# Performance work log

Measured on AMD Instinct MI355X. Metric: run time of the kernel, lower is better.

Reference implementation:

```python
import jax, jax.numpy as jnp
import numpy as np

B, T, C, H = 128, 256, 512, 512

def setup_inputs() -> dict:
    key = jax.random.key(0)
    k1, k2, k3, k4 = jax.random.split(key, 4)
    x = jax.random.normal(k1, (B, T, C), dtype=jnp.float32)
    # nn.Linear(n_embed, H_size, bias=False).weight has shape [H, C]; scaled init
    s = 1.0 / np.sqrt(C)
    Wq = jax.random.normal(k2, (H, C), dtype=jnp.float32) * s
    Wk = jax.random.normal(k3, (H, C), dtype=jnp.float32) * s
    Wv = jax.random.normal(k4, (H, C), dtype=jnp.float32) * s
    return {"x": x, "Wq": Wq, "Wk": Wk, "Wv": Wv}

def reference(x, Wq, Wk, Wv):
    # q,k,v: [B,T,H] = x @ W.T (torch Linear convention)
    q = jnp.einsum('btc,hc->bth', x, Wq)
    k = jnp.einsum('btc,hc->bth', x, Wk)
    v = jnp.einsum('btc,hc->bth', x, Wv)
    scale = k.shape[-1] ** -0.5
    score = jnp.einsum('bqh,bkh->bqk', q, k) * scale  # [B,T,T]
    # causal mask: position j attends to i only if i <= j
    i = jnp.arange(T)
    causal = i[None, :] <= i[:, None]  # [T,T] lower-triangular
    score = jnp.where(causal[None, :, :], score, -jnp.inf)
    attn = jax.nn.softmax(score, axis=-1)
    # dropout is identity in eval mode
    out = jnp.einsum('bqk,bkh->bqh', attn, v)  # [B,T,H]
    return out
```

## Files before the change

### kernel.cpp

```cpp
#include <hip/hip_runtime.h>

#define B_ 128
#define T_ 256
#define C_ 512
#define H_ 512
#define CSCALE 0.063763824f

typedef _Float16 f16x8 __attribute__((ext_vector_type(8)));
typedef _Float16 f16x4 __attribute__((ext_vector_type(4)));
typedef _Float16 f16x2 __attribute__((ext_vector_type(2)));
typedef float    f32x4 __attribute__((ext_vector_type(4)));
typedef float    f32x16 __attribute__((ext_vector_type(16)));
typedef unsigned int u32;
typedef u32 u32x4 __attribute__((ext_vector_type(4)));

__device__ __forceinline__ void gld16(const void* gsrc, void* ldst) {
  __builtin_amdgcn_global_load_lds(
      (__attribute__((address_space(1))) void*)gsrc,
      (__attribute__((address_space(3))) void*)ldst, 16, 0, 0);
}

__global__ __launch_bounds__(256) void cvt_kernel(
    const float4* __restrict__ x, const float4* __restrict__ wq,
    const float4* __restrict__ wk, const float4* __restrict__ wv,
    f16x4* __restrict__ dst) {
  const int NX = (B_ * T_ * C_) / 4;
  const int NW = (H_ * C_) / 4;
  const int total = NX + 3 * NW;
  int gid = blockIdx.x * 256 + threadIdx.x;
  int gsz = gridDim.x * 256;
  for (int i = gid; i < total; i += gsz) {
    float4 f;
    if (i < NX)            f = x[i];
    else if (i < NX + NW)  f = wq[i - NX];
    else if (i < NX + 2*NW) f = wk[i - NX - NW];
    else                   f = wv[i - NX - 2*NW];
    f16x4 u = {(_Float16)f.x, (_Float16)f.y, (_Float16)f.z, (_Float16)f.w};
    dst[i] = u;
  }
}

__global__ __launch_bounds__(512, 2) void proj_kernel(
    const _Float16* __restrict__ xh, const _Float16* __restrict__ wh,
    _Float16* __restrict__ qh, _Float16* __restrict__ kh,
    _Float16* __restrict__ vth) {
  __shared__ _Float16 L[65536];

  const int tid  = threadIdx.x;
  const int lane = tid & 63;
  const int wave = tid >> 6;
  const int lr = lane & 15, lk = lane >> 4;
  const int lane8 = lane * 8;
  const int wr = wave >> 2, wc = wave & 3;
  const int m0 = blockIdx.x * 256;
  const int n0 = blockIdx.y * 256;
  const int z  = blockIdx.z;
  const _Float16* wz = wh + z * (H_ * C_);

  const int srow = wave * 16 + lr;
  const int scol = lk * 8;
  const _Float16* aS = xh + (size_t)(m0 + srow) * C_ + scol;
  const _Float16* bS = wz + (size_t)(n0 + srow) * C_ + scol;

  f32x4 acc[8][4];
#pragma unroll
  for (int i = 0; i < 8; ++i)
#pragma unroll
    for (int j = 0; j < 4; ++j) acc[i][j] = {0.f, 0.f, 0.f, 0.f};
  f16x8 af[4], bf[4];

  gld16(aS,               &L[(wave) * 512]);
  gld16(aS + 65536,       &L[(8 + wave) * 512]);
  gld16(bS,               &L[16384 + (wave) * 512]);
  gld16(bS + 65536,       &L[16384 + (8 + wave) * 512]);
  gld16(aS + 32,          &L[(16 + wave) * 512]);
  gld16(aS + 65536 + 32,  &L[(16 + 8 + wave) * 512]);
  gld16(bS + 32,          &L[16384 + (16 + wave) * 512]);
  gld16(bS + 65536 + 32,  &L[16384 + (16 + 8 + wave) * 512]);
  asm volatile("s_waitcnt vmcnt(4)" ::: "memory");
  __builtin_amdgcn_s_barrier();

#define PH(BUF, MH, KH, STK, SKK, SBUF, SB, VM) do {                          \
    if ((MH) == 0) {                                                           \
      _Pragma("unroll") for (int ni = 0; ni < 4; ++ni)                         \
        bf[ni] = *(const f16x8*)&L[(BUF) * 32768 + 16384 +                     \
                                   ((KH) * 16 + wc * 4 + ni) * 512 + lane8];   \
    }                                                                          \
    _Pragma("unroll") for (int q = 0; q < 4; ++q)                              \
      af[q] = *(const f16x8*)&L[(BUF) * 32768 +                                \
                                ((KH) * 16 + wr * 8 + (MH) * 4 + q) * 512 +    \
                                lane8];                                        \
    {                                                                          \
      const _Float16* s_ = (SB) ? bS : aS;                                     \
      const int db_ = (SBUF) * 32768 + ((SB) ? 16384 : 0);                     \
      gld16(s_ + (STK) + (SKK) * 32,                                           \
            &L[db_ + ((SKK) * 16 + wave) * 512]);                              \
      gld16(s_ + 65536 + (STK) + (SKK) * 32,                                   \
            &L[db_ + ((SKK) * 16 + 8 + wave) * 512]);                          \
    }                                                                          \
    __builtin_amdgcn_s_barrier();                                              \
    __builtin_amdgcn_s_setprio(1);                                             \
    _Pragma("unroll") for (int q = 0; q < 4; ++q)                              \
      _Pragma("unroll") for (int ni = 0; ni < 4; ++ni)                         \
        acc[(MH) * 4 + q][ni] = __builtin_amdgcn_mfma_f32_16x16x32_f16(        \
            af[q], bf[ni], acc[(MH) * 4 + q][ni], 0, 0, 0);                    \
    __builtin_amdgcn_s_setprio(0);                                             \
    if (VM) asm volatile("s_waitcnt vmcnt(4)" ::: "memory");                   \
    __builtin_amdgcn_s_barrier();                                              \
  } while (0)

#pragma unroll 1
  for (int it = 0; it < 4; ++it) {
    const int k1 = (2 * it + 1) * 64;
    const int k2 = (2 * it + 2 < 8 ? 2 * it + 2 : 7) * 64;
    PH(0, 0, 0, k1, 0, 1, 0, 0);
    PH(0, 1, 0, k1, 0, 1, 1, 1);
    PH(0, 0, 1, k1, 1, 1, 0, 0);
    PH(0, 1, 1, k1, 1, 1, 1, 1);
    PH(1, 0, 0, k2, 0, 0, 0, 0);
    PH(1, 1, 0, k2, 0, 0, 1, 1);
    PH(1, 0, 1, k2, 1, 0, 0, 0);
    PH(1, 1, 1, k2, 1, 0, 1, 1);
  }
#undef PH

  if (z < 2) {
    _Float16* out = (z == 0) ? qh : kh;
#pragma unroll
    for (int mi = 0; mi < 8; ++mi) {
      int mg = m0 + wr * 128 + mi * 16 + lk * 4;
#pragma unroll
      for (int ni = 0; ni < 4; ++ni) {
        int n = n0 + wc * 64 + ni * 16 + lr;
#pragma unroll
        for (int r = 0; r < 4; ++r)
          out[(size_t)(mg + r) * H_ + n] = (_Float16)acc[mi][ni][r];
      }
    }
  } else {
    int bb = m0 >> 8;
#pragma unroll
    for (int mi = 0; mi < 8; ++mi) {
      int ttb = wr * 128 + mi * 16 + lk * 4;
#pragma unroll
      for (int ni = 0; ni < 4; ++ni) {
        int n = n0 + wc * 64 + ni * 16 + lr;
        f16x4 u = {(_Float16)acc[mi][ni][0], (_Float16)acc[mi][ni][1],
                   (_Float16)acc[mi][ni][2], (_Float16)acc[mi][ni][3]};
        *(f16x4*)&vth[(size_t)bb * (H_ * T_) + (size_t)n * T_ + ttb] = u;
      }
    }
  }
}

__global__ __launch_bounds__(256, 2) void attn_kernel(
    const _Float16* __restrict__ qh, const _Float16* __restrict__ kh,
    const _Float16* __restrict__ vth, float* __restrict__ dout) {
  __shared__ f32x4 Ex[2][4][4][64];

  const int tid  = threadIdx.x;
  const int lane = tid & 63;
  const int wq   = tid >> 6;
  const int lq   = lane & 31;
  const int hi   = lane >> 5;
  const int flat = blockIdx.x;
  const int xcd  = flat & 7;
  const int rest = flat >> 3;
  const int qb   = 7 - (rest & 7);
  const int g    = rest >> 3;
  const int b    = xcd + (g << 3);
  const int q0   = qb * 32;
  const int nkv  = qb + 1;
  const int hbase = wq * 128;
  const int qg   = q0 + lq;

  f16x8 qf[8];
  const _Float16* qp = qh + ((size_t)b * T_ + qg) * H_ + hbase + hi * 8;
#pragma unroll
  for (int ks = 0; ks < 8; ++ks) qf[ks] = *(const f16x8*)&qp[ks * 16];

  f32x16 ot[4];
#pragma unroll
  for (int i = 0; i < 4; ++i) ot[i] = {};
  float m_ = -1e30f, l_ = 0.f;

  const _Float16* kp = kh  + ((size_t)b * T_ + lq) * H_ + hbase + hi * 8;
  const _Float16* vp = vth + ((size_t)b * H_ + hbase + lq) * T_ + hi * 8;

  for (int kvt = 0; kvt < nkv; ++kvt) {
    const int kv0 = kvt * 32;

    f16x8 kf[8];
#pragma unroll
    for (int ks = 0; ks < 8; ++ks)
      kf[ks] = *(const f16x8*)&kp[(size_t)kv0 * H_ + ks * 16];
    f32x16 st = {};
#pragma unroll
    for (int ks = 0; ks < 8; ++ks)
      st = __builtin_amdgcn_mfma_f32_32x32x16_f16(kf[ks], qf[ks], st, 0, 0, 0);

    const int buf = kvt & 1;
#pragma unroll
    for (int c = 0; c < 4; ++c) {
      f32x4 w4 = {st[c*4+0], st[c*4+1], st[c*4+2], st[c*4+3]};
      Ex[buf][wq][c][lane] = w4;
    }
    __syncthreads();
#pragma unroll
    for (int ow = 0; ow < 4; ++ow) {
      if (ow == wq) continue;
#pragma unroll
      for (int c = 0; c < 4; ++c) {
        f32x4 r4 = Ex[buf][ow][c][lane];
        st[c*4+0] += r4[0]; st[c*4+1] += r4[1];
        st[c*4+2] += r4[2]; st[c*4+3] += r4[3];
      }
    }

    float p[16], rm = -1e30f;
    const int kvb = kv0 + 4 * hi;
#pragma unroll
    for (int r = 0; r < 16; ++r) {
      int kvg = kvb + (r & 3) + 8 * (r >> 2);
      float v = (kvg > qg) ? -1e30f : st[r];
      p[r] = v;
      rm = fmaxf(rm, v);
    }
    rm = fmaxf(rm, __shfl_xor(rm, 32, 64));

    if (__any((int)(rm > m_ + 64.f))) {
      float mn = fmaxf(m_, rm);
      float al = __builtin_amdgcn_exp2f((m_ - mn) * CSCALE);
      m_ = mn; l_ *= al;
#pragma unroll
      for (int i = 0; i < 4; ++i)
#pragma unroll
        for (int e = 0; e < 16; ++e) ot[i][e] *= al;
    }
    float rs = 0.f;
#pragma unroll
    for (int r = 0; r < 16; ++r) {
      p[r] = __builtin_amdgcn_exp2f((p[r] - m_) * CSCALE);
      rs += p[r];
    }
    rs += __shfl_xor(rs, 32, 64);
    l_ += rs;

    u32 w[8], sw[8];
#pragma unroll
    for (int i = 0; i < 8; ++i) {
      f16x2 h2; h2[0] = (_Float16)p[2*i]; h2[1] = (_Float16)p[2*i+1];
      w[i] = __builtin_bit_cast(u32, h2);
    }
#pragma unroll
    for (int i = 0; i < 8; ++i) sw[i] = (u32)__shfl_xor((int)w[i], 32, 64);
    u32x4 t0 = { hi ? sw[2] : w[0],  hi ? sw[3] : w[1],
                 hi ? w[2]  : sw[0], hi ? w[3]  : sw[1] };
    u32x4 t1 = { hi ? sw[6] : w[4],  hi ? sw[7] : w[5],
                 hi ? w[6]  : sw[4], hi ? w[7]  : sw[5] };
    f16x8 pb0 = __builtin_bit_cast(f16x8, t0);
    f16x8 pb1 = __builtin_bit_cast(f16x8, t1);

#pragma unroll
    for (int ht = 0; ht < 4; ++ht) {
      f16x8 va0 = *(const f16x8*)&vp[(size_t)(ht * 32) * T_ + kv0];
      f16x8 va1 = *(const f16x8*)&vp[(size_t)(ht * 32) * T_ + kv0 + 16];
      ot[ht] = __builtin_amdgcn_mfma_f32_32x32x16_f16(va0, pb0, ot[ht], 0, 0, 0);
      ot[ht] = __builtin_amdgcn_mfma_f32_32x32x16_f16(va1, pb1, ot[ht], 0, 0, 0);
    }
  }

  float li = 1.0f / l_;
  float* op = dout + ((size_t)b * T_ + qg) * H_ + hbase + 4 * hi;
#pragma unroll
  for (int ht = 0; ht < 4; ++ht)
#pragma unroll
    for (int rq = 0; rq < 4; ++rq) {
      f32x4 v4 = {ot[ht][rq*4+0] * li, ot[ht][rq*4+1] * li,
                  ot[ht][rq*4+2] * li, ot[ht][rq*4+3] * li};
      *(f32x4*)&op[ht * 32 + rq * 8] = v4;
    }
}

extern "C" void kernel_launch(void* const* d_in, const int* in_sizes, int n_in,
                              void* d_out, int out_size, void* d_ws, size_t ws_size,
                              hipStream_t stream) {
  const size_t NXE = (size_t)B_ * T_ * C_;
  const size_t NWE = (size_t)3 * H_ * C_;
  const size_t NQE = (size_t)B_ * T_ * H_;
  const size_t need = (NXE + NWE + 3 * NQE) * sizeof(_Float16);
  if (ws_size < need) return;

  const float* x  = (const float*)d_in[0];
  const float* wq = (const float*)d_in[1];
  const float* wk = (const float*)d_in[2];
  const float* wv = (const float*)d_in[3];

  _Float16* xh  = (_Float16*)d_ws;
  _Float16* wh  = xh + NXE;
  _Float16* qh  = wh + NWE;
  _Float16* kh  = qh + NQE;
  _Float16* vth = kh + NQE;

  cvt_kernel<<<2048, 256, 0, stream>>>((const float4*)x, (const float4*)wq,
                                       (const float4*)wk, (const float4*)wv,
                                       (f16x4*)xh);
  proj_kernel<<<dim3(128, 2, 3), 512, 0, stream>>>(xh, wh, qh, kh, vth);
  attn_kernel<<<1024, 256, 0, stream>>>(qh, kh, vth, (float*)d_out);
}
```

Before: 171.9 us.

## Software-pipeline QK^T score computation one tile ahead in attention kernel

Restructures the attention loop so the next KV tile's K loads and QK^T MFMAs are issued after the PV MFMAs of the current tile, with partial scores stored into the alternate LDS buffer. The loop then begins with a barrier and a summation of all four waves' partials. It also raises the occupancy hint to 3 blocks per CU, trims register usage in the P packing, and adds s_setprio around MFMA blocks. The goal is to hide K load latency and barrier stalls behind compute, at the cost of register pressure that could spill under the tighter launch bound.

```diff
diff --git a/kernel.cpp b/kernel.cpp
--- a/kernel.cpp
+++ b/kernel.cpp
@@ -153,7 +153,7 @@
   }
 }
 
-__global__ __launch_bounds__(256, 2) void attn_kernel(
+__global__ __launch_bounds__(256, 3) void attn_kernel(
     const _Float16* __restrict__ qh, const _Float16* __restrict__ kh,
     const _Float16* __restrict__ vth, float* __restrict__ dout) {
   __shared__ f32x4 Ex[2][4][4][64];
@@ -187,43 +187,51 @@
   const _Float16* kp = kh  + ((size_t)b * T_ + lq) * H_ + hbase + hi * 8;
   const _Float16* vp = vth + ((size_t)b * H_ + hbase + lq) * T_ + hi * 8;
 
+  f16x8 kf[8];
+#pragma unroll
+  for (int ks = 0; ks < 8; ++ks) kf[ks] = *(const f16x8*)&kp[ks * 16];
+  {
+    f32x16 s2 = {};
+#pragma unroll
+    for (int ks = 0; ks < 8; ++ks)
+      s2 = __builtin_amdgcn_mfma_f32_32x32x16_f16(kf[ks], qf[ks], s2, 0, 0, 0);
+#pragma unroll
+    for (int c = 0; c < 4; ++c) {
+      f32x4 w4 = {s2[c*4+0], s2[c*4+1], s2[c*4+2], s2[c*4+3]};
+      Ex[0][wq][c][lane] = w4;
+    }
+  }
+
   for (int kvt = 0; kvt < nkv; ++kvt) {
     const int kv0 = kvt * 32;
-
-    f16x8 kf[8];
-#pragma unroll
-    for (int ks = 0; ks < 8; ++ks)
-      kf[ks] = *(const f16x8*)&kp[(size_t)kv0 * H_ + ks * 16];
-    f32x16 st = {};
-#pragma unroll
-    for (int ks = 0; ks < 8; ++ks)
-      st = __builtin_amdgcn_mfma_f32_32x32x16_f16(kf[ks], qf[ks], st, 0, 0, 0);
-
     const int buf = kvt & 1;
+    const bool more = (kvt + 1 < nkv);
+    __syncthreads();
+
+    f32x16 st;
 #pragma unroll
     for (int c = 0; c < 4; ++c) {
-      f32x4 w4 = {st[c*4+0], st[c*4+1], st[c*4+2], st[c*4+3]};
-      Ex[buf][wq][c][lane] = w4;
-    }
-    __syncthreads();
-#pragma unroll
-    for (int ow = 0; ow < 4; ++ow) {
-      if (ow == wq) continue;
-#pragma unroll
-      for (int c = 0; c < 4; ++c) {
-        f32x4 r4 = Ex[buf][ow][c][lane];
-        st[c*4+0] += r4[0]; st[c*4+1] += r4[1];
-        st[c*4+2] += r4[2]; st[c*4+3] += r4[3];
-      }
-    }
-
-    float p[16], rm = -1e30f;
+      f32x4 r0 = Ex[buf][0][c][lane];
+      f32x4 r1 = Ex[buf][1][c][lane];
+      f32x4 r2 = Ex[buf][2][c][lane];
+      f32x4 r3 = Ex[buf][3][c][lane];
+      f32x4 r = (r0 + r1) + (r2 + r3);
+      st[c*4+0] = r[0]; st[c*4+1] = r[1]; st[c*4+2] = r[2]; st[c*4+3] = r[3];
+    }
+
+    if (more) {
+#pragma unroll
+      for (int ks = 0; ks < 8; ++ks)
+        kf[ks] = *(const f16x8*)&kp[(size_t)(kv0 + 32) * H_ + ks * 16];
+    }
+
+    float rm = -1e30f;
     const int kvb = kv0 + 4 * hi;
 #pragma unroll
     for (int r = 0; r < 16; ++r) {
       int kvg = kvb + (r & 3) + 8 * (r >> 2);
       float v = (kvg > qg) ? -1e30f : st[r];
-      p[r] = v;
+      st[r] = v;
       rm = fmaxf(rm, v);
     }
     rm = fmaxf(rm, __shfl_xor(rm, 32, 64));
@@ -240,33 +248,64 @@
     float rs = 0.f;
 #pragma unroll
     for (int r = 0; r < 16; ++r) {
-      p[r] = __builtin_amdgcn_exp2f((p[r] - m_) * CSCALE);
-      rs += p[r];
+      st[r] = __builtin_amdgcn_exp2f((st[r] - m_) * CSCALE);
+      rs += st[r];
     }
     rs += __shfl_xor(rs, 32, 64);
     l_ += rs;
 
-    u32 w[8], sw[8];
-#pragma unroll
-    for (int i = 0; i < 8; ++i) {
-      f16x2 h2; h2[0] = (_Float16)p[2*i]; h2[1] = (_Float16)p[2*i+1];
-      w[i] = __builtin_bit_cast(u32, h2);
-    }
-#pragma unroll
-    for (int i = 0; i < 8; ++i) sw[i] = (u32)__shfl_xor((int)w[i], 32, 64);
-    u32x4 t0 = { hi ? sw[2] : w[0],  hi ? sw[3] : w[1],
-                 hi ? w[2]  : sw[0], hi ? w[3]  : sw[1] };
-    u32x4 t1 = { hi ? sw[6] : w[4],  hi ? sw[7] : w[5],
-                 hi ? w[6]  : sw[4], hi ? w[7]  : sw[5] };
-    f16x8 pb0 = __builtin_bit_cast(f16x8, t0);
-    f16x8 pb1 = __builtin_bit_cast(f16x8, t1);
-
+    f16x8 pb0, pb1;
+    {
+      f16x2 h0 = {(_Float16)st[0], (_Float16)st[1]};
+      f16x2 h1 = {(_Float16)st[2], (_Float16)st[3]};
+      f16x2 h2 = {(_Float16)st[4], (_Float16)st[5]};
+      f16x2 h3 = {(_Float16)st[6], (_Float16)st[7]};
+      u32 w0 = __builtin_bit_cast(u32, h0), w1 = __builtin_bit_cast(u32, h1);
+      u32 w2 = __builtin_bit_cast(u32, h2), w3 = __builtin_bit_cast(u32, h3);
+      u32 s0 = (u32)__shfl_xor((int)w0, 32, 64);
+      u32 s1 = (u32)__shfl_xor((int)w1, 32, 64);
+      u32 s2 = (u32)__shfl_xor((int)w2, 32, 64);
+      u32 s3 = (u32)__shfl_xor((int)w3, 32, 64);
+      u32x4 t0 = { hi ? s2 : w0, hi ? s3 : w1, hi ? w2 : s0, hi ? w3 : s1 };
+      pb0 = __builtin_bit_cast(f16x8, t0);
+    }
+    {
+      f16x2 h0 = {(_Float16)st[8],  (_Float16)st[9]};
+      f16x2 h1 = {(_Float16)st[10], (_Float16)st[11]};
+      f16x2 h2 = {(_Float16)st[12], (_Float16)st[13]};
+      f16x2 h3 = {(_Float16)st[14], (_Float16)st[15]};
+      u32 w0 = __builtin_bit_cast(u32, h0), w1 = __builtin_bit_cast(u32, h1);
+      u32 w2 = __builtin_bit_cast(u32, h2), w3 = __builtin_bit_cast(u32, h3);
+      u32 s0 = (u32)__shfl_xor((int)w0, 32, 64);
+      u32 s1 = (u32)__shfl_xor((int)w1, 32, 64);
+      u32 s2 = (u32)__shfl_xor((int)w2, 32, 64);
+      u32 s3 = (u32)__shfl_xor((int)w3, 32, 64);
+      u32x4 t1 = { hi ? s2 : w0, hi ? s3 : w1, hi ? w2 : s0, hi ? w3 : s1 };
+      pb1 = __builtin_bit_cast(f16x8, t1);
+    }
+
+    __builtin_amdgcn_s_setprio(1);
 #pragma unroll
     for (int ht = 0; ht < 4; ++ht) {
       f16x8 va0 = *(const f16x8*)&vp[(size_t)(ht * 32) * T_ + kv0];
       f16x8 va1 = *(const f16x8*)&vp[(size_t)(ht * 32) * T_ + kv0 + 16];
       ot[ht] = __builtin_amdgcn_mfma_f32_32x32x16_f16(va0, pb0, ot[ht], 0, 0, 0);
       ot[ht] = __builtin_amdgcn_mfma_f32_32x32x16_f16(va1, pb1, ot[ht], 0, 0, 0);
+    }
+    __builtin_amdgcn_s_setprio(0);
+
+    if (more) {
+      f32x16 s2v = {};
+      __builtin_amdgcn_s_setprio(1);
+#pragma unroll
+      for (int ks = 0; ks < 8; ++ks)
+        s2v = __builtin_amdgcn_mfma_f32_32x32x16_f16(kf[ks], qf[ks], s2v, 0, 0, 0);
+      __builtin_amdgcn_s_setprio(0);
+#pragma unroll
+      for (int c = 0; c < 4; ++c) {
+        f32x4 w4 = {s2v[c*4+0], s2v[c*4+1], s2v[c*4+2], s2v[c*4+3]};
+        Ex[buf ^ 1][wq][c][lane] = w4;
+      }
     }
   }
 
```

Result: slower. 206.2 us (+20.0%).
